# Optimization experiments

Hardware: AMD Instinct MI355X
Metric: run time of the kernel (lower is better)

## Reference

```python
import jax, jax.numpy as jnp
import numpy as np
import math

C = 512
GROUPS = 32
EPS = 1e-06


def group_norm(x, w, b):
    # x: [B, C, H, W]; 32 groups over channels
    B, Cc, H, W = x.shape
    xg = x.reshape(B, GROUPS, Cc // GROUPS, H, W)
    mu = jnp.mean(xg, axis=(2, 3, 4), keepdims=True)
    var = jnp.var(xg, axis=(2, 3, 4), keepdims=True)
    xn = ((xg - mu) * jax.lax.rsqrt(var + EPS)).reshape(B, Cc, H, W)
    return xn * w[None, :, None, None] + b[None, :, None, None]


def setup_inputs() -> dict:
    key = jax.random.key(0)
    ks = jax.random.split(key, 7)
    B, H, W = 2, 64, 64
    x = jax.random.normal(ks[0], (B, C, H, W), dtype=jnp.float32)
    gn_w = jnp.ones((C,), dtype=jnp.float32)
    gn_b = jnp.zeros((C,), dtype=jnp.float32)
    s = 1.0 / math.sqrt(C)
    qkv_w = jax.random.normal(ks[1], (3 * C, C), dtype=jnp.float32) * s
    qkv_b = jnp.zeros((3 * C,), dtype=jnp.float32)
    proj_w = jax.random.normal(ks[2], (C, C), dtype=jnp.float32) * s
    proj_b = jnp.zeros((C,), dtype=jnp.float32)
    return {"x": x, "gn_w": gn_w, "gn_b": gn_b, "qkv_w": qkv_w,
            "qkv_b": qkv_b, "proj_w": proj_w, "proj_b": proj_b}


def reference(x, gn_w, gn_b, qkv_w, qkv_b, proj_w, proj_b):
    residue = x
    B, Cc, H, W = x.shape
    N = H * W
    constant = 1.0 / math.sqrt(Cc)
    xn = group_norm(x, gn_w, gn_b)
    # 1x1 conv == channel matmul
    qkv = jnp.einsum('bchw,oc->bohw', xn, qkv_w) + qkv_b[None, :, None, None]
    q, k, v = jnp.split(qkv, 3, axis=1)
    q = q.reshape(B, Cc, N)
    k = k.reshape(B, Cc, N)
    v = v.reshape(B, Cc, N)
    # attn[b,i,j] = sum_c k[b,c,i] * q[b,c,j]   (k^T @ q, per original code)
    attn = jnp.einsum('bci,bcj->bij', k, q) * constant
    soft = jax.nn.softmax(attn, axis=2)  # softmax over q-index j, as in torch dim=2
    # output[b,c,i] = sum_j v[b,c,j] * soft[b,j,i]   (v @ soft)
    out = jnp.einsum('bcj,bji->bci', v, soft).reshape(B, Cc, H, W)
    proj = jnp.einsum('bchw,oc->bohw', out, proj_w) + proj_b[None, :, None, None]
    return residue + proj
```

## Files before the change

kernel.cpp:

```cpp
#include <hip/hip_runtime.h>
#include <hip/hip_bf16.h>
#include <math.h>

typedef unsigned short ushort_t;
typedef __attribute__((ext_vector_type(8))) unsigned short ushort8;
typedef __attribute__((ext_vector_type(4))) unsigned short ushort4_t;
typedef __attribute__((ext_vector_type(8))) __bf16 bf16x8;
typedef __attribute__((ext_vector_type(4))) float f32x4;

__device__ inline ushort_t f2b(float f) {
  __hip_bfloat16 h = __float2bfloat16(f);
  return __builtin_bit_cast(ushort_t, h);
}
__device__ inline float b2f(ushort_t u) {
  __hip_bfloat16 h = __builtin_bit_cast(__hip_bfloat16, u);
  return __bfloat162float(h);
}

__device__ inline void gload16(const ushort_t* g, ushort_t* l) {
  __builtin_amdgcn_global_load_lds(
      (const __attribute__((address_space(1))) unsigned int*)g,
      (__attribute__((address_space(3))) unsigned int*)l, 16, 0, 0);
}

__device__ inline void xcd_swz(int& bx, int& by, int& bz) {
  const int nx = gridDim.x, ny = gridDim.y;
  const int nwg = nx * ny * gridDim.z;
  const int orig = blockIdx.x + nx * (blockIdx.y + ny * blockIdx.z);
  const int q = nwg >> 3, r = nwg & 7, xcd = orig & 7, loc = orig >> 3;
  const int wg = (xcd < r ? xcd * (q + 1) : r * (q + 1) + (xcd - r) * q) + loc;
  bx = wg % nx;
  by = (wg / nx) % ny;
  bz = wg / (nx * ny);
}

__global__ __launch_bounds__(256) void prep_weights(
    const float* __restrict__ qkv_w, const float* __restrict__ proj_w,
    ushort_t* __restrict__ qkvw, ushort_t* __restrict__ projw) {
  int idx = blockIdx.x * 256 + threadIdx.x;
  const int NQ = 1536 * 512;
  if (idx < NQ) {
    qkvw[idx] = f2b(qkv_w[idx]);
  } else {
    int j = idx - NQ;
    if (j < 512 * 512) projw[j] = f2b(proj_w[j]);
  }
}

__global__ __launch_bounds__(256) void gn_stats(const float* __restrict__ x,
                                                float* __restrict__ stats) {
  const int tid = threadIdx.x;
  const int bg = blockIdx.x;
  const float4* xv = (const float4*)(x + (size_t)bg * 65536);
  float s = 0.f, ss = 0.f;
  for (int i = tid; i < 16384; i += 256) {
    float4 v = xv[i];
    s += v.x + v.y + v.z + v.w;
    ss += v.x * v.x + v.y * v.y + v.z * v.z + v.w * v.w;
  }
  __shared__ float red[8];
  for (int off = 32; off > 0; off >>= 1) {
    s += __shfl_down(s, off);
    ss += __shfl_down(ss, off);
  }
  if ((tid & 63) == 0) { red[tid >> 6] = s; red[4 + (tid >> 6)] = ss; }
  __syncthreads();
  if (tid == 0) {
    float st = red[0] + red[1] + red[2] + red[3];
    float sst = red[4] + red[5] + red[6] + red[7];
    float mean = st * (1.f / 65536.f);
    float var = sst * (1.f / 65536.f) - mean * mean;
    stats[bg * 2] = mean;
    stats[bg * 2 + 1] = rsqrtf(var + 1e-6f);
  }
}

__global__ __launch_bounds__(256) void gn_apply_t(
    const float* __restrict__ x, const float* __restrict__ w,
    const float* __restrict__ bgn, const float* __restrict__ stats,
    ushort_t* __restrict__ xnT) {
  __shared__ ushort_t tile[64][68];
  const int b = blockIdx.z;
  const int p0 = blockIdx.x * 64, c0 = blockIdx.y * 64;
  const int tid = threadIdx.x;
  const float* xb = x + ((size_t)b * 512 + c0) * 4096 + p0;
  const int tc = tid >> 4, tp = (tid & 15) * 4;
#pragma unroll
  for (int pass = 0; pass < 4; ++pass) {
    int c = pass * 16 + tc;
    int cg = c0 + c;
    float mean = stats[(b * 32 + (cg >> 4)) * 2];
    float inv = stats[(b * 32 + (cg >> 4)) * 2 + 1];
    float wc = w[cg] * inv;
    float bc = bgn[cg] - mean * wc;
    float4 v = *(const float4*)(xb + (size_t)c * 4096 + tp);
    tile[c][tp] = f2b(v.x * wc + bc);
    tile[c][tp + 1] = f2b(v.y * wc + bc);
    tile[c][tp + 2] = f2b(v.z * wc + bc);
    tile[c][tp + 3] = f2b(v.w * wc + bc);
  }
  __syncthreads();
  const int c8 = (tid & 7) * 8;
#pragma unroll
  for (int pass = 0; pass < 2; ++pass) {
    int p = pass * 32 + (tid >> 3);
    ushort8 u;
#pragma unroll
    for (int e = 0; e < 8; ++e) u[e] = tile[c8 + e][p];
    *(ushort8*)(xnT + ((size_t)b * 4096 + p0 + p) * 512 + c0 + c8) = u;
  }
}

template <int EPI>
__global__ __launch_bounds__(512, 2) void gemm8(
    const ushort_t* __restrict__ A, const ushort_t* __restrict__ B,
    void* __restrict__ Cg, const float* __restrict__ bias,
    float* __restrict__ smp, int N, int K, int lda, int ldb, size_t sA,
    size_t sB, size_t sC, float scale) {
  __shared__ __align__(16) ushort_t Al[2][256 * 64];
  __shared__ __align__(16) ushort_t Bl[2][256 * 64];
  __shared__ float s_max[2][256], s_sum[2][256];

  int bx, by, bz;
  xcd_swz(bx, by, bz);
  const ushort_t* Ab = A + bz * sA;
  const ushort_t* Bb = B + bz * sB;
  const int bm0 = by * 256, bn0 = bx * 256;
  const int tid = threadIdx.x;
  const int w = tid >> 6, lane = tid & 63;
  const int wr = w >> 2, wc = w & 3;
  const int fr = lane & 15, fq = lane >> 4;

  const int srow = tid >> 3, scb = tid & 7;
  const int ssw = scb ^ (srow & 7);
  const ushort_t* aS = Ab + (size_t)(bm0 + srow) * lda + ssw * 8;
  const ushort_t* bS = Bb + (size_t)(bn0 + srow) * ldb + ssw * 8;

  auto stage_a = [&](int s, int kk) {
#pragma unroll
    for (int g = 0; g < 4; ++g)
      gload16(aS + (size_t)(g * 64) * lda + kk, &Al[s][g * 4096 + w * 512]);
  };
  auto stage_b = [&](int s, int kk) {
#pragma unroll
    for (int g = 0; g < 4; ++g)
      gload16(bS + (size_t)(g * 64) * ldb + kk, &Bl[s][g * 4096 + w * 512]);
  };

  f32x4 acc[8][4] = {};
  bf16x8 a_r[4][2], b_r[4][2];

  auto read_a = [&](int s, int mh) {
#pragma unroll
    for (int mi = 0; mi < 4; ++mi) {
      int row = wr * 128 + mh * 64 + mi * 16 + fr;
#pragma unroll
      for (int ks = 0; ks < 2; ++ks) {
        int blk = ((ks * 4 + fq) ^ (row & 7)) * 8;
        a_r[mi][ks] = *(const bf16x8*)&Al[s][row * 64 + blk];
      }
    }
  };
  auto read_b = [&](int s, int nh) {
#pragma unroll
    for (int ni = 0; ni < 2; ++ni) {
      int row = wc * 64 + nh * 32 + ni * 16 + fr;
#pragma unroll
      for (int ks = 0; ks < 2; ++ks) {
        int blk = ((ks * 4 + fq) ^ (row & 7)) * 8;
        b_r[nh * 2 + ni][ks] = *(const bf16x8*)&Bl[s][row * 64 + blk];
      }
    }
  };
  auto phase_mfma = [&](int mh, int nh) {
    __builtin_amdgcn_s_setprio(1);
#pragma unroll
    for (int ks = 0; ks < 2; ++ks)
#pragma unroll
      for (int mi = 0; mi < 4; ++mi)
#pragma unroll
        for (int ni = 0; ni < 2; ++ni)
          acc[mh * 4 + mi][nh * 2 + ni] =
              __builtin_amdgcn_mfma_f32_16x16x32_bf16(
                  a_r[mi][ks], b_r[nh * 2 + ni][ks],
                  acc[mh * 4 + mi][nh * 2 + ni], 0, 0, 0);
    __builtin_amdgcn_s_setprio(0);
  };

  const int nt = K >> 6;
  stage_b(0, 0);
  stage_a(0, 0);
  if (nt > 1) {
    stage_b(1, 64);
    stage_a(1, 64);
    asm volatile("s_waitcnt vmcnt(8)" ::: "memory");
  } else {
    asm volatile("s_waitcnt vmcnt(0)" ::: "memory");
  }
  __builtin_amdgcn_s_barrier();

  for (int t = 0; t < nt; ++t) {
    const int s = t & 1;
    const int kk2 = (t + 2) << 6;
    const bool st2 = (t + 2) < nt;
    read_a(s, 0);
    read_b(s, 0);
    __builtin_amdgcn_s_barrier();
    phase_mfma(0, 0);
    __builtin_amdgcn_s_barrier();
    read_b(s, 1);
    __builtin_amdgcn_s_barrier();
    phase_mfma(0, 1);
    __builtin_amdgcn_s_barrier();
    read_a(s, 1);
    asm volatile("" ::: "memory");
    if (st2) stage_b(s, kk2);
    __builtin_amdgcn_s_barrier();
    phase_mfma(1, 0);
    __builtin_amdgcn_s_barrier();
    asm volatile("" ::: "memory");
    if (st2) stage_a(s, kk2);
    __builtin_amdgcn_s_barrier();
    phase_mfma(1, 1);
    if (st2)
      asm volatile("s_waitcnt vmcnt(8)" ::: "memory");
    else if (t + 1 < nt)
      asm volatile("s_waitcnt vmcnt(0)" ::: "memory");
    __builtin_amdgcn_s_barrier();
  }

  const size_t cbase = (size_t)bz * sC;
#pragma unroll
  for (int mi = 0; mi < 8; ++mi) {
#pragma unroll
    for (int r = 0; r < 4; ++r) {
      int gm = bm0 + wr * 128 + mi * 16 + fq * 4 + r;
#pragma unroll
      for (int ni = 0; ni < 4; ++ni) {
        int gn = bn0 + wc * 64 + ni * 16 + fr;
        float v = acc[mi][ni][r];
        size_t off = cbase + (size_t)gm * N + gn;
        if constexpr (EPI == 0) {
          ((ushort_t*)Cg)[off] = f2b(v + bias[gn]);
        } else if constexpr (EPI == 2) {
          ((ushort_t*)Cg)[off] = f2b(__expf(fminf(v * scale, 80.f)));
        }
      }
    }
  }

  if constexpr (EPI == 2) {
    float cm[4], cs4[4];
#pragma unroll
    for (int ni = 0; ni < 4; ++ni) {
      float m = -3e38f;
#pragma unroll
      for (int mi = 0; mi < 8; ++mi)
#pragma unroll
        for (int r = 0; r < 4; ++r) m = fmaxf(m, acc[mi][ni][r] * scale);
      m = fmaxf(m, __shfl_xor(m, 16));
      m = fmaxf(m, __shfl_xor(m, 32));
      float s = 0.f;
#pragma unroll
      for (int mi = 0; mi < 8; ++mi)
#pragma unroll
        for (int r = 0; r < 4; ++r) s += __expf(acc[mi][ni][r] * scale - m);
      s += __shfl_xor(s, 16);
      s += __shfl_xor(s, 32);
      cm[ni] = m;
      cs4[ni] = s;
    }
    __syncthreads();
    if (lane < 16) {
#pragma unroll
      for (int ni = 0; ni < 4; ++ni) {
        s_max[wr][wc * 64 + ni * 16 + lane] = cm[ni];
        s_sum[wr][wc * 64 + ni * 16 + lane] = cs4[ni];
      }
    }
    __syncthreads();
    if (tid < 256) {
      float m0 = s_max[0][tid], m1 = s_max[1][tid];
      float M = fmaxf(m0, m1);
      float S = s_sum[0][tid] * __expf(m0 - M) + s_sum[1][tid] * __expf(m1 - M);
      size_t o = (((size_t)bz * 16 + by) * 4096 + bn0 + tid) * 2;
      smp[o] = M;
      smp[o + 1] = S;
    }
  }
}

template <int EPI>
__global__ __launch_bounds__(256) void gemm_bt(
    const ushort_t* __restrict__ A, const ushort_t* __restrict__ B,
    void* __restrict__ Cg, const float* __restrict__ colsc, int N, int K,
    int lda, int ldb, size_t sA, size_t sB, size_t sC) {
  __shared__ __align__(16) ushort_t As[2][4096];
  __shared__ __align__(16) ushort_t Bs[2][4096];
  int bx, by, bz;
  xcd_swz(bx, by, bz);
  const ushort_t* Ab = A + bz * sA;
  const ushort_t* Bb = B + bz * sB;
  const int bm0 = by * 128, bn0 = bx * 128;
  const int tid = threadIdx.x;
  const int w = tid >> 6, lane = tid & 63;
  const int sm = tid >> 2, sk = (tid & 3) * 8;
  const ushort_t* aS = Ab + (size_t)(bm0 + sm) * lda + sk;
  const ushort_t* bS = Bb + (size_t)(bn0 + sm) * ldb + sk;
  const int wm = (w >> 1) * 64, wn = (w & 1) * 64;
  const int fr = lane & 15, fk = (lane >> 4) * 8;
  f32x4 acc[4][4] = {};

  auto stage = [&](int buf, int kk) {
    ushort_t* la = &As[buf][w * 512];
    ushort_t* lb = &Bs[buf][w * 512];
    gload16(aS + kk, la);
    gload16(aS + (size_t)64 * lda + kk, la + 2048);
    gload16(bS + kk, lb);
    gload16(bS + (size_t)64 * ldb + kk, lb + 2048);
  };

  stage(0, 0);
  __syncthreads();
  const int nt = K >> 5;
  for (int t = 0; t < nt; ++t) {
    const int cur = t & 1;
    if (t + 1 < nt) stage(cur ^ 1, (t + 1) << 5);
    bf16x8 af[4], bfv[4];
#pragma unroll
    for (int mi = 0; mi < 4; mi++)
      af[mi] = *(const bf16x8*)&As[cur][(wm + mi * 16 + fr) * 32 + fk];
#pragma unroll
    for (int ni = 0; ni < 4; ni++)
      bfv[ni] = *(const bf16x8*)&Bs[cur][(wn + ni * 16 + fr) * 32 + fk];
#pragma unroll
    for (int mi = 0; mi < 4; mi++)
#pragma unroll
      for (int ni = 0; ni < 4; ni++)
        acc[mi][ni] = __builtin_amdgcn_mfma_f32_16x16x32_bf16(
            af[mi], bfv[ni], acc[mi][ni], 0, 0, 0);
    __syncthreads();
  }

  const int r0 = (lane >> 4) * 4;
  const size_t cbase = (size_t)bz * sC;
#pragma unroll
  for (int mi = 0; mi < 4; mi++) {
#pragma unroll
    for (int r = 0; r < 4; r++) {
      int gm = bm0 + wm + mi * 16 + r0 + r;
#pragma unroll
      for (int ni = 0; ni < 4; ni++) {
        int gn = bn0 + wn + ni * 16 + fr;
        float v = acc[mi][ni][r];
        size_t off = cbase + (size_t)gm * N + gn;
        if constexpr (EPI == 3) {
          ((ushort_t*)Cg)[off] = f2b(v * colsc[(size_t)bz * 4096 + gn]);
        } else {
          ((ushort_t*)Cg)[off] = f2b(v);
        }
      }
    }
  }
}

__global__ __launch_bounds__(256) void sm_fin(const float* __restrict__ part,
                                              float* __restrict__ alpha) {
  int idx = blockIdx.x * 256 + threadIdx.x;
  int b = idx >> 12, j = idx & 4095;
  float M = -3e38f, S = 0.f;
#pragma unroll
  for (int rc = 0; rc < 16; rc++) {
    size_t o = (((size_t)b * 16 + rc) * 4096 + j) * 2;
    float mi = part[o], si = part[o + 1];
    float nm = fmaxf(M, mi);
    S = S * __expf(M - nm) + si * __expf(mi - nm);
    M = nm;
  }
  alpha[idx] = __expf(-M) / S;
}

__global__ __launch_bounds__(256) void finalize(
    const ushort_t* __restrict__ outT, const float* __restrict__ x,
    const float* __restrict__ pb, float* __restrict__ out) {
  __shared__ ushort_t tile[64][72];
  const int b = blockIdx.z;
  const int p0 = blockIdx.x * 64, o0 = blockIdx.y * 64;
  const int tid = threadIdx.x;
  const int tp = tid >> 2, to = (tid & 3) * 16;
  const ushort8* src =
      (const ushort8*)(outT + ((size_t)b * 4096 + p0 + tp) * 512 + o0 + to);
  ushort8 u0 = src[0], u1 = src[1];
  *(ushort8*)&tile[tp][to] = u0;
  *(ushort8*)&tile[tp][to + 8] = u1;
  __syncthreads();
  const int wo = tid >> 2, wp = (tid & 3) * 16;
  float bias = pb[o0 + wo];
  const float* xr = x + ((size_t)b * 512 + o0 + wo) * 4096 + p0 + wp;
  float* orow = out + ((size_t)b * 512 + o0 + wo) * 4096 + p0 + wp;
#pragma unroll
  for (int e = 0; e < 16; ++e)
    orow[e] = b2f(tile[wp + e][wo]) + xr[e] + bias;
}

extern "C" void kernel_launch(void* const* d_in, const int* in_sizes, int n_in,
                              void* d_out, int out_size, void* d_ws,
                              size_t ws_size, hipStream_t stream) {
  const float* x = (const float*)d_in[0];
  const float* gn_w = (const float*)d_in[1];
  const float* gn_b = (const float*)d_in[2];
  const float* qkv_w = (const float*)d_in[3];
  const float* qkv_b = (const float*)d_in[4];
  const float* proj_w = (const float*)d_in[5];
  const float* proj_b = (const float*)d_in[6];
  float* out = (float*)d_out;

  char* ws = (char*)d_ws;
  ushort_t* xnT   = (ushort_t*)(ws);
  ushort_t* Wpp   = (ushort_t*)(ws);
  ushort_t* qkvw  = (ushort_t*)(ws + 8388608);
  ushort_t* projw = (ushort_t*)(ws + 9961472);
  float*    stats = (float*)(ws + 10485760);
  ushort_t* qkvT  = (ushort_t*)(ws + 10486272);
  ushort_t* outT  = (ushort_t*)(ws + 10486272);
  ushort_t* P     = (ushort_t*)(ws + 35652096);
  float*    smp   = (float*)(ws + 102760960);
  float*    alpha = (float*)(ws + 104858112);

  const float scale = 0.04419417382415922f;
  const size_t sXN = 2097152, sQKV = (size_t)4096 * 1536, sP = 16777216;

  prep_weights<<<4096, 256, 0, stream>>>(qkv_w, proj_w, qkvw, projw);
  gn_stats<<<64, 256, 0, stream>>>(x, stats);
  gn_apply_t<<<dim3(64, 8, 2), 256, 0, stream>>>(x, gn_w, gn_b, stats, xnT);
  gemm8<0><<<dim3(6, 32, 1), 512, 0, stream>>>(
      xnT, qkvw, qkvT, qkv_b, nullptr, 1536, 512, 512, 512, 0, 0, 0, 1.f);
  gemm8<2><<<dim3(16, 16, 2), 512, 0, stream>>>(
      qkvT, qkvT + 512, P, nullptr, smp, 4096, 512, 1536, 1536, sQKV, sQKV,
      sP, scale);
  sm_fin<<<32, 256, 0, stream>>>(smp, alpha);
  gemm_bt<3><<<dim3(32, 4, 2), 256, 0, stream>>>(
      projw, qkvT + 1024, Wpp, alpha, 4096, 512, 512, 1536, 0, sQKV, sXN);
  gemm_bt<5><<<dim3(4, 32, 2), 256, 0, stream>>>(
      P, Wpp, outT, nullptr, 512, 4096, 4096, 4096, sP, sXN, sXN);
  finalize<<<dim3(64, 8, 2), 256, 0, stream>>>(outT, x, proj_b, out);
}
```

Before: 214.4 us.

## Replace gemm_bt with swizzled 3-stage pipelined GEMM and reuse it for QKV

The simple double-buffered 128x128 GEMM becomes gemm_pl. It uses a BK=64 tile with an XOR-swizzled LDS layout to cut bank conflicts and keeps two loads in flight via vmcnt waits. MFMAs run under split s_setprio phases so the next prefetch is issued mid-compute. The QKV projection moves from the 256x? gemm8 kernel to gemm_pl with 128x128 tiles on more blocks, which raises parallelism at the cost of more redundant operand loads.

```diff
diff --git a/kernel.cpp b/kernel.cpp
--- a/kernel.cpp
+++ b/kernel.cpp
@@ -4,7 +4,6 @@
 
 typedef unsigned short ushort_t;
 typedef __attribute__((ext_vector_type(8))) unsigned short ushort8;
-typedef __attribute__((ext_vector_type(4))) unsigned short ushort4_t;
 typedef __attribute__((ext_vector_type(8))) __bf16 bf16x8;
 typedef __attribute__((ext_vector_type(4))) float f32x4;
 
@@ -240,11 +239,7 @@
         int gn = bn0 + wc * 64 + ni * 16 + fr;
         float v = acc[mi][ni][r];
         size_t off = cbase + (size_t)gm * N + gn;
-        if constexpr (EPI == 0) {
-          ((ushort_t*)Cg)[off] = f2b(v + bias[gn]);
-        } else if constexpr (EPI == 2) {
-          ((ushort_t*)Cg)[off] = f2b(__expf(fminf(v * scale, 80.f)));
-        }
+        ((ushort_t*)Cg)[off] = f2b(__expf(fminf(v * scale, 80.f)));
       }
     }
   }
@@ -291,12 +286,13 @@
 }
 
 template <int EPI>
-__global__ __launch_bounds__(256) void gemm_bt(
+__global__ __launch_bounds__(256) void gemm_pl(
     const ushort_t* __restrict__ A, const ushort_t* __restrict__ B,
-    void* __restrict__ Cg, const float* __restrict__ colsc, int N, int K,
-    int lda, int ldb, size_t sA, size_t sB, size_t sC) {
-  __shared__ __align__(16) ushort_t As[2][4096];
-  __shared__ __align__(16) ushort_t Bs[2][4096];
+    void* __restrict__ Cg, const float* __restrict__ bias,
+    const float* __restrict__ colsc, int N, int K, int lda, int ldb,
+    size_t sA, size_t sB, size_t sC) {
+  __shared__ __align__(16) ushort_t Al[2][128 * 64];
+  __shared__ __align__(16) ushort_t Bl[2][128 * 64];
   int bx, by, bz;
   xcd_swz(bx, by, bz);
   const ushort_t* Ab = A + bz * sA;
@@ -304,42 +300,84 @@
   const int bm0 = by * 128, bn0 = bx * 128;
   const int tid = threadIdx.x;
   const int w = tid >> 6, lane = tid & 63;
-  const int sm = tid >> 2, sk = (tid & 3) * 8;
-  const ushort_t* aS = Ab + (size_t)(bm0 + sm) * lda + sk;
-  const ushort_t* bS = Bb + (size_t)(bn0 + sm) * ldb + sk;
   const int wm = (w >> 1) * 64, wn = (w & 1) * 64;
-  const int fr = lane & 15, fk = (lane >> 4) * 8;
+  const int fr = lane & 15, fq = lane >> 4;
+
+  const int srow = tid >> 3, scb = tid & 7;
+  const int ssw = scb ^ (srow & 7);
+  const ushort_t* aS = Ab + (size_t)(bm0 + srow) * lda + ssw * 8;
+  const ushort_t* bS = Bb + (size_t)(bn0 + srow) * ldb + ssw * 8;
+
+  auto stage = [&](int s, int kk) {
+#pragma unroll
+    for (int g = 0; g < 4; ++g)
+      gload16(aS + (size_t)(g * 32) * lda + kk, &Al[s][g * 2048 + w * 512]);
+#pragma unroll
+    for (int g = 0; g < 4; ++g)
+      gload16(bS + (size_t)(g * 32) * ldb + kk, &Bl[s][g * 2048 + w * 512]);
+  };
+
   f32x4 acc[4][4] = {};
-
-  auto stage = [&](int buf, int kk) {
-    ushort_t* la = &As[buf][w * 512];
-    ushort_t* lb = &Bs[buf][w * 512];
-    gload16(aS + kk, la);
-    gload16(aS + (size_t)64 * lda + kk, la + 2048);
-    gload16(bS + kk, lb);
-    gload16(bS + (size_t)64 * ldb + kk, lb + 2048);
-  };
-
+  bf16x8 a_r[4][2], b_r[4][2];
+
+  const int nt = K >> 6;
   stage(0, 0);
-  __syncthreads();
-  const int nt = K >> 5;
+  if (nt > 1) {
+    stage(1, 64);
+    asm volatile("s_waitcnt vmcnt(8)" ::: "memory");
+  } else {
+    asm volatile("s_waitcnt vmcnt(0)" ::: "memory");
+  }
+  __builtin_amdgcn_s_barrier();
+
   for (int t = 0; t < nt; ++t) {
-    const int cur = t & 1;
-    if (t + 1 < nt) stage(cur ^ 1, (t + 1) << 5);
-    bf16x8 af[4], bfv[4];
-#pragma unroll
-    for (int mi = 0; mi < 4; mi++)
-      af[mi] = *(const bf16x8*)&As[cur][(wm + mi * 16 + fr) * 32 + fk];
-#pragma unroll
-    for (int ni = 0; ni < 4; ni++)
-      bfv[ni] = *(const bf16x8*)&Bs[cur][(wn + ni * 16 + fr) * 32 + fk];
-#pragma unroll
-    for (int mi = 0; mi < 4; mi++)
-#pragma unroll
-      for (int ni = 0; ni < 4; ni++)
-        acc[mi][ni] = __builtin_amdgcn_mfma_f32_16x16x32_bf16(
-            af[mi], bfv[ni], acc[mi][ni], 0, 0, 0);
-    __syncthreads();
+    const int s = t & 1;
+#pragma unroll
+    for (int mi = 0; mi < 4; ++mi) {
+      int row = wm + mi * 16 + fr;
+#pragma unroll
+      for (int ks = 0; ks < 2; ++ks) {
+        int blk = ((ks * 4 + fq) ^ (row & 7)) * 8;
+        a_r[mi][ks] = *(const bf16x8*)&Al[s][row * 64 + blk];
+      }
+    }
+#pragma unroll
+    for (int ni = 0; ni < 4; ++ni) {
+      int row = wn + ni * 16 + fr;
+#pragma unroll
+      for (int ks = 0; ks < 2; ++ks) {
+        int blk = ((ks * 4 + fq) ^ (row & 7)) * 8;
+        b_r[ni][ks] = *(const bf16x8*)&Bl[s][row * 64 + blk];
+      }
+    }
+    __builtin_amdgcn_s_barrier();
+    __builtin_amdgcn_s_setprio(1);
+#pragma unroll
+    for (int ks = 0; ks < 2; ++ks)
+#pragma unroll
+      for (int mi = 0; mi < 4; ++mi)
+#pragma unroll
+        for (int ni = 0; ni < 2; ++ni)
+          acc[mi][ni] = __builtin_amdgcn_mfma_f32_16x16x32_bf16(
+              a_r[mi][ks], b_r[ni][ks], acc[mi][ni], 0, 0, 0);
+    __builtin_amdgcn_s_setprio(0);
+    __builtin_amdgcn_s_barrier();
+    if (t + 2 < nt) stage(s, (t + 2) << 6);
+    __builtin_amdgcn_s_setprio(1);
+#pragma unroll
+    for (int ks = 0; ks < 2; ++ks)
+#pragma unroll
+      for (int mi = 0; mi < 4; ++mi)
+#pragma unroll
+        for (int ni = 2; ni < 4; ++ni)
+          acc[mi][ni] = __builtin_amdgcn_mfma_f32_16x16x32_bf16(
+              a_r[mi][ks], b_r[ni][ks], acc[mi][ni], 0, 0, 0);
+    __builtin_amdgcn_s_setprio(0);
+    if (t + 2 < nt)
+      asm volatile("s_waitcnt vmcnt(8)" ::: "memory");
+    else if (t + 1 < nt)
+      asm volatile("s_waitcnt vmcnt(0)" ::: "memory");
+    __builtin_amdgcn_s_barrier();
   }
 
   const int r0 = (lane >> 4) * 4;
@@ -354,7 +392,9 @@
         int gn = bn0 + wn + ni * 16 + fr;
         float v = acc[mi][ni][r];
         size_t off = cbase + (size_t)gm * N + gn;
-        if constexpr (EPI == 3) {
+        if constexpr (EPI == 0) {
+          ((ushort_t*)Cg)[off] = f2b(v + bias[gn]);
+        } else if constexpr (EPI == 3) {
           ((ushort_t*)Cg)[off] = f2b(v * colsc[(size_t)bz * 4096 + gn]);
         } else {
           ((ushort_t*)Cg)[off] = f2b(v);
@@ -433,15 +473,16 @@
   prep_weights<<<4096, 256, 0, stream>>>(qkv_w, proj_w, qkvw, projw);
   gn_stats<<<64, 256, 0, stream>>>(x, stats);
   gn_apply_t<<<dim3(64, 8, 2), 256, 0, stream>>>(x, gn_w, gn_b, stats, xnT);
-  gemm8<0><<<dim3(6, 32, 1), 512, 0, stream>>>(
-      xnT, qkvw, qkvT, qkv_b, nullptr, 1536, 512, 512, 512, 0, 0, 0, 1.f);
+  gemm_pl<0><<<dim3(12, 64, 1), 256, 0, stream>>>(
+      xnT, qkvw, qkvT, qkv_b, nullptr, 1536, 512, 512, 512, 0, 0, 0);
   gemm8<2><<<dim3(16, 16, 2), 512, 0, stream>>>(
       qkvT, qkvT + 512, P, nullptr, smp, 4096, 512, 1536, 1536, sQKV, sQKV,
       sP, scale);
   sm_fin<<<32, 256, 0, stream>>>(smp, alpha);
-  gemm_bt<3><<<dim3(32, 4, 2), 256, 0, stream>>>(
-      projw, qkvT + 1024, Wpp, alpha, 4096, 512, 512, 1536, 0, sQKV, sXN);
-  gemm_bt<5><<<dim3(4, 32, 2), 256, 0, stream>>>(
-      P, Wpp, outT, nullptr, 512, 4096, 4096, 4096, sP, sXN, sXN);
+  gemm_pl<3><<<dim3(32, 4, 2), 256, 0, stream>>>(
+      projw, qkvT + 1024, Wpp, nullptr, alpha, 4096, 512, 512, 1536, 0, sQKV,
+      sXN);
+  gemm_pl<5><<<dim3(4, 32, 2), 256, 0, stream>>>(
+      P, Wpp, outT, nullptr, nullptr, 512, 4096, 4096, 4096, sP, sXN, sXN);
   finalize<<<dim3(64, 8, 2), 256, 0, stream>>>(outT, x, proj_b, out);
 }
```

New measurement: 190.4 us. 1.13x faster.
